# Optimization experiments

Hardware: AMD Instinct MI355X
Metric: run time of the kernel (lower is better)

Reference implementation:

```python
import jax, jax.numpy as jnp
import numpy as np

EMBED_DIM = 1024
NUM_HEADS = 16
HEAD_DIM = EMBED_DIM // NUM_HEADS


def setup_inputs() -> dict:
    key = jax.random.key(0)
    k1, k2, k3, k4, k5 = jax.random.split(key, 5)
    B, L, C = 4, 4096, EMBED_DIM
    s = 1.0 / np.sqrt(C)
    return {
        "x": jax.random.normal(k1, (B, L, C), dtype=jnp.float32),
        "qkv_w": jax.random.normal(k2, (3 * C, C), dtype=jnp.float32) * s,
        "qkv_b": jax.random.normal(k3, (3 * C,), dtype=jnp.float32) * 0.01,
        "out_w": jax.random.normal(k4, (C, C), dtype=jnp.float32) * s,
        "out_b": jax.random.normal(k5, (C,), dtype=jnp.float32) * 0.01,
        "num_frames": 16,
    }


def reference(x, qkv_w, qkv_b, out_w, out_b, num_frames):
    B, L, C = x.shape
    P = L // num_frames  # patches per frame
    H, D = NUM_HEADS, HEAD_DIM
    xf = x.reshape(B * num_frames, P, C)
    # fused QKV projection (torch Linear: y = x @ W^T + b)
    qkv = xf @ qkv_w.T + qkv_b                      # [BF, P, 3C]
    qkv = qkv.reshape(B * num_frames, P, 3, H, D)
    qkv = jnp.transpose(qkv, (2, 0, 3, 1, 4))        # [3, BF, H, P, D]
    q, k, v = qkv[0], qkv[1], qkv[2]
    scores = jnp.einsum("bhqd,bhkd->bhqk", q, k) / np.sqrt(D)
    attn = jax.nn.softmax(scores, axis=-1)
    out = jnp.einsum("bhqk,bhkd->bhqd", attn, v)     # [BF, H, P, D]
    out = jnp.transpose(out, (0, 2, 1, 3)).reshape(B, L, C)
    return out @ out_w.T + out_b
```

## Files before the change

### kernel.cpp

```cpp
#include <hip/hip_runtime.h>


typedef __bf16 bf16x8 __attribute__((ext_vector_type(8)));
typedef float f32x4 __attribute__((ext_vector_type(4)));

__device__ __forceinline__ void gload_lds16(const void* g, void* l) {
  __builtin_amdgcn_global_load_lds(
      (__attribute__((address_space(1))) void*)(g),
      (__attribute__((address_space(3))) void*)(l), 16, 0, 0);
}

__global__ __launch_bounds__(256) void cvt_f32_bf16(
    const float* __restrict__ in, __bf16* __restrict__ out, int n8) {
  int i = blockIdx.x * 256 + threadIdx.x;
  if (i >= n8) return;
  const float4* p = (const float4*)in;
  float4 a = p[2 * i];
  float4 b = p[2 * i + 1];
  bf16x8 v;
  v[0] = (__bf16)a.x; v[1] = (__bf16)a.y; v[2] = (__bf16)a.z; v[3] = (__bf16)a.w;
  v[4] = (__bf16)b.x; v[5] = (__bf16)b.y; v[6] = (__bf16)b.z; v[7] = (__bf16)b.w;
  ((bf16x8*)out)[i] = v;
}

template <bool BF16_OUT>
__global__ __launch_bounds__(512, 2) void gemm256(
    const __bf16* __restrict__ A, const __bf16* __restrict__ Bm,
    const float* __restrict__ bias, void* __restrict__ Cv,
    int M, int N, int K) {
  __shared__ alignas(16) __bf16 Al[2][256 * 64];
  __shared__ alignas(16) __bf16 Bl[2][256 * 64];

  const int tid = threadIdx.x, lane = tid & 63, wid = tid >> 6;
  const int wr = wid >> 2, wc = wid & 3;
  const int l15 = lane & 15, l4 = lane >> 4;

  const int nwg = gridDim.x * gridDim.y;
  const int bid = blockIdx.y * gridDim.x + blockIdx.x;
  const int q = nwg >> 3;
  const int swz = (bid & 7) * q + (bid >> 3);
  const int bn = swz % gridDim.x, bm = swz / gridDim.x;

  const int NT = K >> 6;

  const __bf16* gA[4];
  const __bf16* gB[4];
#pragma unroll
  for (int c = 0; c < 4; ++c) {
    int seg = c * 512 + tid;
    int row = seg >> 3, bl = (seg & 7) ^ (row & 7);
    gA[c] = A + (size_t)(bm * 256 + row) * K + bl * 8;
    gB[c] = Bm + (size_t)(bn * 256 + row) * K + bl * 8;
  }

#define STAGE(b)                                         \
  {                                                      \
    _Pragma("unroll") for (int c = 0; c < 4; ++c) {      \
      gload_lds16(gA[c], &Al[b][(c * 512 + tid) * 8]);   \
      gA[c] += 64;                                       \
    }                                                    \
    _Pragma("unroll") for (int c = 0; c < 4; ++c) {      \
      gload_lds16(gB[c], &Bl[b][(c * 512 + tid) * 8]);   \
      gB[c] += 64;                                       \
    }                                                    \
  }

  const int rsw = l15 & 7;
  const int pk0 = ((l4) ^ rsw) * 8;
  const int pk1 = ((4 + l4) ^ rsw) * 8;
  const int aRow = (wr * 128 + l15) * 64;
  const int bRow = (wc * 64 + l15) * 64;

  f32x4 acc[8][4] = {};

  STAGE(0);
  STAGE(1);
  asm volatile("s_waitcnt vmcnt(8)" ::: "memory");
  __builtin_amdgcn_s_barrier();

  for (int t = 0; t < NT; ++t) {
    const __bf16* Ab = &Al[t & 1][0];
    const __bf16* Bb = &Bl[t & 1][0];
    const bool hasStage = (t + 2 < NT);
    const bool hasNext = (t + 1 < NT);

    bf16x8 b0 = *(const bf16x8*)(Bb + bRow + 0 * 1024 + pk0);
    bf16x8 b1 = *(const bf16x8*)(Bb + bRow + 1 * 1024 + pk0);
    bf16x8 b2 = *(const bf16x8*)(Bb + bRow + 2 * 1024 + pk0);
    bf16x8 b3 = *(const bf16x8*)(Bb + bRow + 3 * 1024 + pk0);
    bf16x8 x0 = *(const bf16x8*)(Ab + aRow + 0 * 1024 + pk0);
    bf16x8 x1 = *(const bf16x8*)(Ab + aRow + 1 * 1024 + pk0);
    bf16x8 x2 = *(const bf16x8*)(Ab + aRow + 2 * 1024 + pk0);
    bf16x8 x3 = *(const bf16x8*)(Ab + aRow + 3 * 1024 + pk0);
    __builtin_amdgcn_s_setprio(1);
#pragma unroll
    for (int n = 0; n < 4; ++n) {
      bf16x8 bb = n == 0 ? b0 : n == 1 ? b1 : n == 2 ? b2 : b3;
      acc[0][n] = __builtin_amdgcn_mfma_f32_16x16x32_bf16(x0, bb, acc[0][n], 0, 0, 0);
      acc[1][n] = __builtin_amdgcn_mfma_f32_16x16x32_bf16(x1, bb, acc[1][n], 0, 0, 0);
      acc[2][n] = __builtin_amdgcn_mfma_f32_16x16x32_bf16(x2, bb, acc[2][n], 0, 0, 0);
      acc[3][n] = __builtin_amdgcn_mfma_f32_16x16x32_bf16(x3, bb, acc[3][n], 0, 0, 0);
    }
    __builtin_amdgcn_s_setprio(0);

    x0 = *(const bf16x8*)(Ab + aRow + 4 * 1024 + pk0);
    x1 = *(const bf16x8*)(Ab + aRow + 5 * 1024 + pk0);
    x2 = *(const bf16x8*)(Ab + aRow + 6 * 1024 + pk0);
    x3 = *(const bf16x8*)(Ab + aRow + 7 * 1024 + pk0);
    __builtin_amdgcn_s_setprio(1);
#pragma unroll
    for (int n = 0; n < 4; ++n) {
      bf16x8 bb = n == 0 ? b0 : n == 1 ? b1 : n == 2 ? b2 : b3;
      acc[4][n] = __builtin_amdgcn_mfma_f32_16x16x32_bf16(x0, bb, acc[4][n], 0, 0, 0);
      acc[5][n] = __builtin_amdgcn_mfma_f32_16x16x32_bf16(x1, bb, acc[5][n], 0, 0, 0);
      acc[6][n] = __builtin_amdgcn_mfma_f32_16x16x32_bf16(x2, bb, acc[6][n], 0, 0, 0);
      acc[7][n] = __builtin_amdgcn_mfma_f32_16x16x32_bf16(x3, bb, acc[7][n], 0, 0, 0);
    }
    __builtin_amdgcn_s_setprio(0);

    b0 = *(const bf16x8*)(Bb + bRow + 0 * 1024 + pk1);
    b1 = *(const bf16x8*)(Bb + bRow + 1 * 1024 + pk1);
    b2 = *(const bf16x8*)(Bb + bRow + 2 * 1024 + pk1);
    b3 = *(const bf16x8*)(Bb + bRow + 3 * 1024 + pk1);
    x0 = *(const bf16x8*)(Ab + aRow + 0 * 1024 + pk1);
    x1 = *(const bf16x8*)(Ab + aRow + 1 * 1024 + pk1);
    x2 = *(const bf16x8*)(Ab + aRow + 2 * 1024 + pk1);
    x3 = *(const bf16x8*)(Ab + aRow + 3 * 1024 + pk1);
    __builtin_amdgcn_s_setprio(1);
#pragma unroll
    for (int n = 0; n < 4; ++n) {
      bf16x8 bb = n == 0 ? b0 : n == 1 ? b1 : n == 2 ? b2 : b3;
      acc[0][n] = __builtin_amdgcn_mfma_f32_16x16x32_bf16(x0, bb, acc[0][n], 0, 0, 0);
      acc[1][n] = __builtin_amdgcn_mfma_f32_16x16x32_bf16(x1, bb, acc[1][n], 0, 0, 0);
      acc[2][n] = __builtin_amdgcn_mfma_f32_16x16x32_bf16(x2, bb, acc[2][n], 0, 0, 0);
      acc[3][n] = __builtin_amdgcn_mfma_f32_16x16x32_bf16(x3, bb, acc[3][n], 0, 0, 0);
    }
    __builtin_amdgcn_s_setprio(0);

    x0 = *(const bf16x8*)(Ab + aRow + 4 * 1024 + pk1);
    x1 = *(const bf16x8*)(Ab + aRow + 5 * 1024 + pk1);
    x2 = *(const bf16x8*)(Ab + aRow + 6 * 1024 + pk1);
    x3 = *(const bf16x8*)(Ab + aRow + 7 * 1024 + pk1);
    asm volatile("s_waitcnt lgkmcnt(0)" ::: "memory");
    __builtin_amdgcn_sched_barrier(0);
    __builtin_amdgcn_s_barrier();
    if (hasStage) STAGE(t & 1);
    __builtin_amdgcn_s_setprio(1);
#pragma unroll
    for (int n = 0; n < 4; ++n) {
      bf16x8 bb = n == 0 ? b0 : n == 1 ? b1 : n == 2 ? b2 : b3;
      acc[4][n] = __builtin_amdgcn_mfma_f32_16x16x32_bf16(x0, bb, acc[4][n], 0, 0, 0);
      acc[5][n] = __builtin_amdgcn_mfma_f32_16x16x32_bf16(x1, bb, acc[5][n], 0, 0, 0);
      acc[6][n] = __builtin_amdgcn_mfma_f32_16x16x32_bf16(x2, bb, acc[6][n], 0, 0, 0);
      acc[7][n] = __builtin_amdgcn_mfma_f32_16x16x32_bf16(x3, bb, acc[7][n], 0, 0, 0);
    }
    __builtin_amdgcn_s_setprio(0);
    if (hasNext) {
      if (hasStage)
        asm volatile("s_waitcnt vmcnt(8)" ::: "memory");
      else
        asm volatile("s_waitcnt vmcnt(0)" ::: "memory");
      __builtin_amdgcn_s_barrier();
    }
  }
#undef STAGE

  const int r0 = l4 * 4;
#pragma unroll
  for (int m = 0; m < 8; ++m) {
#pragma unroll
    for (int n = 0; n < 4; ++n) {
      int row = bm * 256 + wr * 128 + m * 16 + r0;
      int col = bn * 256 + wc * 64 + n * 16 + l15;
      float bb = bias[col];
#pragma unroll
      for (int r = 0; r < 4; ++r) {
        float v = acc[m][n][r] + bb;
        if (BF16_OUT)
          ((__bf16*)Cv)[(size_t)(row + r) * N + col] = (__bf16)v;
        else
          ((float*)Cv)[(size_t)(row + r) * N + col] = v;
      }
    }
  }
}

__global__ __launch_bounds__(256, 2) void attn_kernel(
    const __bf16* __restrict__ qkv, __bf16* __restrict__ attnOut) {
  __shared__ alignas(16) __bf16 Ks[256 * 64];
  __shared__ alignas(16) __bf16 Vt[64 * 256];
  __shared__ alignas(16) __bf16 Pl[4][64 * 32];

  const int h = blockIdx.x, bf = blockIdx.y;
  const int tid = threadIdx.x, lane = tid & 63, wid = tid >> 6;
  const int l15 = lane & 15, l4 = lane >> 4;

  const __bf16* base = qkv + (size_t)(bf * 256) * 3072 + h * 64;

#pragma unroll
  for (int rr = 0; rr < 8; ++rr) {
    int s = rr * 256 + wid * 64 + lane;
    int r = s >> 3, t = s & 7, c8 = t ^ (r & 7);
    gload_lds16(base + 1024 + (size_t)r * 3072 + c8 * 8, &Ks[s * 8]);
  }

  {
    const __bf16* vrow = base + 2048 + (size_t)tid * 3072;
    bf16x8 vv[8];
#pragma unroll
    for (int b8 = 0; b8 < 8; ++b8) vv[b8] = *(const bf16x8*)(vrow + b8 * 8);
#pragma unroll
    for (int b8 = 0; b8 < 8; ++b8)
#pragma unroll
      for (int e = 0; e < 8; ++e) {
        int d = b8 * 8 + e;
        Vt[d * 256 + (((tid >> 3) ^ (d & 7)) * 8) + (tid & 7)] = vv[b8][e];
      }
  }

  bf16x8 aq[4][2];
  const __bf16* qbase = base + (size_t)(wid * 64) * 3072;
#pragma unroll
  for (int m = 0; m < 4; ++m)
#pragma unroll
    for (int kk = 0; kk < 2; ++kk)
      aq[m][kk] =
          *(const bf16x8*)(qbase + (size_t)(m * 16 + l15) * 3072 + kk * 32 + l4 * 8);

  __syncthreads();

  float m_run[4][4], l_run[4][4];
#pragma unroll
  for (int m = 0; m < 4; ++m)
#pragma unroll
    for (int r = 0; r < 4; ++r) { m_run[m][r] = -3.0e38f; l_run[m][r] = 0.f; }
  f32x4 o[4][4] = {};

  __bf16* Pw = &Pl[wid][0];

  for (int jt = 0; jt < 8; ++jt) {
    f32x4 s[4][2] = {};
#pragma unroll
    for (int kk = 0; kk < 2; ++kk) {
      bf16x8 bk[2];
#pragma unroll
      for (int n = 0; n < 2; ++n) {
        int j = jt * 32 + n * 16 + l15;
        int c8 = kk * 4 + l4;
        bk[n] = *(const bf16x8*)&Ks[(j * 8 + (c8 ^ (j & 7))) * 8];
      }
#pragma unroll
      for (int m = 0; m < 4; ++m)
#pragma unroll
        for (int n = 0; n < 2; ++n)
          s[m][n] = __builtin_amdgcn_mfma_f32_16x16x32_bf16(aq[m][kk], bk[n],
                                                            s[m][n], 0, 0, 0);
    }
#pragma unroll
    for (int m = 0; m < 4; ++m)
#pragma unroll
      for (int r = 0; r < 4; ++r) {
        float a0 = s[m][0][r] * 0.125f, a1 = s[m][1][r] * 0.125f;
        float t = fmaxf(a0, a1);
        t = fmaxf(t, __shfl_xor(t, 1));
        t = fmaxf(t, __shfl_xor(t, 2));
        t = fmaxf(t, __shfl_xor(t, 4));
        t = fmaxf(t, __shfl_xor(t, 8));
        float mn = fmaxf(m_run[m][r], t);
        float al = __expf(m_run[m][r] - mn);
        m_run[m][r] = mn;
        float p0 = __expf(a0 - mn), p1 = __expf(a1 - mn);
        s[m][0][r] = p0; s[m][1][r] = p1;
        float rs = p0 + p1;
        rs += __shfl_xor(rs, 1);
        rs += __shfl_xor(rs, 2);
        rs += __shfl_xor(rs, 4);
        rs += __shfl_xor(rs, 8);
        l_run[m][r] = l_run[m][r] * al + rs;
#pragma unroll
        for (int nd = 0; nd < 4; ++nd) o[m][nd][r] *= al;
      }
#pragma unroll
    for (int m = 0; m < 4; ++m)
#pragma unroll
      for (int n = 0; n < 2; ++n)
#pragma unroll
        for (int r = 0; r < 4; ++r) {
          int q = m * 16 + l4 * 4 + r;
          int j = n * 16 + l15;
          Pw[q * 32 + (((j >> 3) ^ (q & 3)) * 8) + (j & 7)] = (__bf16)s[m][n][r];
        }
    bf16x8 ap[4];
#pragma unroll
    for (int m = 0; m < 4; ++m) {
      int q = m * 16 + l15;
      ap[m] = *(const bf16x8*)&Pw[q * 32 + ((l4 ^ (q & 3)) * 8)];
    }
    bf16x8 bv[4];
#pragma unroll
    for (int nd = 0; nd < 4; ++nd) {
      int d = nd * 16 + l15;
      int jb = jt * 4 + l4;
      bv[nd] = *(const bf16x8*)&Vt[d * 256 + ((jb ^ (d & 7)) * 8)];
    }
#pragma unroll
    for (int m = 0; m < 4; ++m)
#pragma unroll
      for (int nd = 0; nd < 4; ++nd)
        o[m][nd] = __builtin_amdgcn_mfma_f32_16x16x32_bf16(ap[m], bv[nd],
                                                           o[m][nd], 0, 0, 0);
  }

  __bf16* ob = attnOut + (size_t)(bf * 256 + wid * 64) * 1024 + h * 64;
#pragma unroll
  for (int m = 0; m < 4; ++m)
#pragma unroll
    for (int r = 0; r < 4; ++r) {
      float inv = 1.0f / l_run[m][r];
#pragma unroll
      for (int nd = 0; nd < 4; ++nd)
        ob[(size_t)(m * 16 + l4 * 4 + r) * 1024 + nd * 16 + l15] =
            (__bf16)(o[m][nd][r] * inv);
    }
}

extern "C" void kernel_launch(void* const* d_in, const int* in_sizes, int n_in,
                              void* d_out, int out_size, void* d_ws,
                              size_t ws_size, hipStream_t stream) {
  const float* x = (const float*)d_in[0];
  const float* qkv_w = (const float*)d_in[1];
  const float* qkv_b = (const float*)d_in[2];
  const float* out_w = (const float*)d_in[3];
  const float* out_b = (const float*)d_in[4];
  float* out = (float*)d_out;

  __bf16* xb = (__bf16*)d_ws;
  __bf16* qkvwb = xb + 16777216;
  __bf16* outwb = qkvwb + 3145728;
  __bf16* qkvb = outwb + 1048576;
  __bf16* attnb = qkvb + (size_t)16384 * 3072;

  cvt_f32_bf16<<<8192, 256, 0, stream>>>(x, xb, 16777216 / 8);
  cvt_f32_bf16<<<1536, 256, 0, stream>>>(qkv_w, qkvwb, 3145728 / 8);
  cvt_f32_bf16<<<512, 256, 0, stream>>>(out_w, outwb, 1048576 / 8);

  gemm256<true><<<dim3(12, 64), 512, 0, stream>>>(xb, qkvwb, qkv_b, qkvb,
                                                  16384, 3072, 1024);

  attn_kernel<<<dim3(16, 64), 256, 0, stream>>>(qkvb, attnb);

  gemm256<false><<<dim3(4, 64), 512, 0, stream>>>(attnb, outwb, out_b, out,
                                                  16384, 1024, 1024);
}
```

Before: 379.1 us.

## Widen attention key tiles, defer row-sum reduction, and use lazy softmax rescaling

The attention inner loop now handles 64 keys per iteration instead of 32, which halves the number of max-reduction and rescale rounds. The running row sum is kept per lane and reduced across lanes only once at the end, rather than shuffled every iteration. Rescaling of the output accumulator is skipped unless some row max grows by more than 8, a lazy-rescale trick that keeps results exact but lets exponents reach up to e^8 before correction. MFMA sections are wrapped in s_setprio to favour matrix issue, at the cost of more registers for the larger score tile.

```diff
diff --git a/kernel.cpp b/kernel.cpp
--- a/kernel.cpp
+++ b/kernel.cpp
@@ -229,86 +229,113 @@
 
   __syncthreads();
 
-  float m_run[4][4], l_run[4][4];
+  float m_run[4][4], lsum[4][4];
 #pragma unroll
   for (int m = 0; m < 4; ++m)
 #pragma unroll
-    for (int r = 0; r < 4; ++r) { m_run[m][r] = -3.0e38f; l_run[m][r] = 0.f; }
+    for (int r = 0; r < 4; ++r) { m_run[m][r] = -3.0e38f; lsum[m][r] = 0.f; }
   f32x4 o[4][4] = {};
 
   __bf16* Pw = &Pl[wid][0];
 
-  for (int jt = 0; jt < 8; ++jt) {
-    f32x4 s[4][2] = {};
+  for (int jt = 0; jt < 4; ++jt) {
+    f32x4 s[4][4] = {};
 #pragma unroll
     for (int kk = 0; kk < 2; ++kk) {
-      bf16x8 bk[2];
-#pragma unroll
-      for (int n = 0; n < 2; ++n) {
-        int j = jt * 32 + n * 16 + l15;
+      bf16x8 bk[4];
+#pragma unroll
+      for (int n = 0; n < 4; ++n) {
+        int j = jt * 64 + n * 16 + l15;
         int c8 = kk * 4 + l4;
         bk[n] = *(const bf16x8*)&Ks[(j * 8 + (c8 ^ (j & 7))) * 8];
       }
+      __builtin_amdgcn_s_setprio(1);
 #pragma unroll
       for (int m = 0; m < 4; ++m)
 #pragma unroll
-        for (int n = 0; n < 2; ++n)
+        for (int n = 0; n < 4; ++n)
           s[m][n] = __builtin_amdgcn_mfma_f32_16x16x32_bf16(aq[m][kk], bk[n],
                                                             s[m][n], 0, 0, 0);
+      __builtin_amdgcn_s_setprio(0);
     }
 #pragma unroll
     for (int m = 0; m < 4; ++m)
 #pragma unroll
+      for (int n = 0; n < 4; ++n) s[m][n] *= 0.125f;
+    float tloc[4][4];
+    float grow = 0.f;
+#pragma unroll
+    for (int m = 0; m < 4; ++m)
+#pragma unroll
       for (int r = 0; r < 4; ++r) {
-        float a0 = s[m][0][r] * 0.125f, a1 = s[m][1][r] * 0.125f;
-        float t = fmaxf(a0, a1);
+        float t = fmaxf(fmaxf(s[m][0][r], s[m][1][r]),
+                        fmaxf(s[m][2][r], s[m][3][r]));
         t = fmaxf(t, __shfl_xor(t, 1));
         t = fmaxf(t, __shfl_xor(t, 2));
         t = fmaxf(t, __shfl_xor(t, 4));
         t = fmaxf(t, __shfl_xor(t, 8));
-        float mn = fmaxf(m_run[m][r], t);
-        float al = __expf(m_run[m][r] - mn);
-        m_run[m][r] = mn;
-        float p0 = __expf(a0 - mn), p1 = __expf(a1 - mn);
-        s[m][0][r] = p0; s[m][1][r] = p1;
-        float rs = p0 + p1;
-        rs += __shfl_xor(rs, 1);
-        rs += __shfl_xor(rs, 2);
-        rs += __shfl_xor(rs, 4);
-        rs += __shfl_xor(rs, 8);
-        l_run[m][r] = l_run[m][r] * al + rs;
-#pragma unroll
-        for (int nd = 0; nd < 4; ++nd) o[m][nd][r] *= al;
-      }
+        tloc[m][r] = t;
+        grow = fmaxf(grow, t - m_run[m][r]);
+      }
+    if (__any(grow > 8.0f)) {
+#pragma unroll
+      for (int m = 0; m < 4; ++m)
+#pragma unroll
+        for (int r = 0; r < 4; ++r) {
+          float mn = fmaxf(m_run[m][r], tloc[m][r]);
+          float al = __expf(m_run[m][r] - mn);
+          m_run[m][r] = mn;
+          lsum[m][r] *= al;
+#pragma unroll
+          for (int nd = 0; nd < 4; ++nd) o[m][nd][r] *= al;
+        }
+    }
 #pragma unroll
     for (int m = 0; m < 4; ++m)
 #pragma unroll
-      for (int n = 0; n < 2; ++n)
-#pragma unroll
-        for (int r = 0; r < 4; ++r) {
-          int q = m * 16 + l4 * 4 + r;
-          int j = n * 16 + l15;
-          Pw[q * 32 + (((j >> 3) ^ (q & 3)) * 8) + (j & 7)] = (__bf16)s[m][n][r];
-        }
-    bf16x8 ap[4];
-#pragma unroll
-    for (int m = 0; m < 4; ++m) {
-      int q = m * 16 + l15;
-      ap[m] = *(const bf16x8*)&Pw[q * 32 + ((l4 ^ (q & 3)) * 8)];
-    }
-    bf16x8 bv[4];
-#pragma unroll
-    for (int nd = 0; nd < 4; ++nd) {
-      int d = nd * 16 + l15;
-      int jb = jt * 4 + l4;
-      bv[nd] = *(const bf16x8*)&Vt[d * 256 + ((jb ^ (d & 7)) * 8)];
-    }
-#pragma unroll
-    for (int m = 0; m < 4; ++m)
-#pragma unroll
-      for (int nd = 0; nd < 4; ++nd)
-        o[m][nd] = __builtin_amdgcn_mfma_f32_16x16x32_bf16(ap[m], bv[nd],
-                                                           o[m][nd], 0, 0, 0);
+      for (int r = 0; r < 4; ++r) {
+        float p0 = __expf(s[m][0][r] - m_run[m][r]);
+        float p1 = __expf(s[m][1][r] - m_run[m][r]);
+        float p2 = __expf(s[m][2][r] - m_run[m][r]);
+        float p3 = __expf(s[m][3][r] - m_run[m][r]);
+        s[m][0][r] = p0; s[m][1][r] = p1; s[m][2][r] = p2; s[m][3][r] = p3;
+        lsum[m][r] += (p0 + p1) + (p2 + p3);
+      }
+#pragma unroll
+    for (int hh = 0; hh < 2; ++hh) {
+#pragma unroll
+      for (int m = 0; m < 4; ++m)
+#pragma unroll
+        for (int nn = 0; nn < 2; ++nn)
+#pragma unroll
+          for (int r = 0; r < 4; ++r) {
+            int qr = m * 16 + l4 * 4 + r;
+            int j = nn * 16 + l15;
+            Pw[qr * 32 + (((j >> 3) ^ (qr & 3)) * 8) + (j & 7)] =
+                (__bf16)s[m][2 * hh + nn][r];
+          }
+      bf16x8 ap[4];
+#pragma unroll
+      for (int m = 0; m < 4; ++m) {
+        int qr = m * 16 + l15;
+        ap[m] = *(const bf16x8*)&Pw[qr * 32 + ((l4 ^ (qr & 3)) * 8)];
+      }
+      bf16x8 bv[4];
+#pragma unroll
+      for (int nd = 0; nd < 4; ++nd) {
+        int d = nd * 16 + l15;
+        int jb = jt * 8 + hh * 4 + l4;
+        bv[nd] = *(const bf16x8*)&Vt[d * 256 + ((jb ^ (d & 7)) * 8)];
+      }
+      __builtin_amdgcn_s_setprio(1);
+#pragma unroll
+      for (int m = 0; m < 4; ++m)
+#pragma unroll
+        for (int nd = 0; nd < 4; ++nd)
+          o[m][nd] = __builtin_amdgcn_mfma_f32_16x16x32_bf16(ap[m], bv[nd],
+                                                             o[m][nd], 0, 0, 0);
+      __builtin_amdgcn_s_setprio(0);
+    }
   }
 
   __bf16* ob = attnOut + (size_t)(bf * 256 + wid * 64) * 1024 + h * 64;
@@ -316,7 +343,12 @@
   for (int m = 0; m < 4; ++m)
 #pragma unroll
     for (int r = 0; r < 4; ++r) {
-      float inv = 1.0f / l_run[m][r];
+      float rs = lsum[m][r];
+      rs += __shfl_xor(rs, 1);
+      rs += __shfl_xor(rs, 2);
+      rs += __shfl_xor(rs, 4);
+      rs += __shfl_xor(rs, 8);
+      float inv = 1.0f / rs;
 #pragma unroll
       for (int nd = 0; nd < 4; ++nd)
         ob[(size_t)(m * 16 + l4 * 4 + r) * 1024 + nd * 16 + l15] =
```

New measurement: 358.6 us. 1.06x faster.
